# Kernel optimization log

Measured on AMD Instinct MI355X. Metric: run time of the kernel, lower is better.

## Reference

```python
import jax, jax.numpy as jnp
import numpy as np
from jax import lax

E, C, N = 3, 2, 2048          # edge types, channels, nodes (= nb_items)
B, T = 64, 50                 # batch, max_seq_length
W_IN = 256; W_OUT = 256; U = 512  # gcn in/out, rnn_units


def setup_inputs() -> dict:
    key = jax.random.key(0)
    ks = jax.random.split(key, 16)
    # sparse-ish adjacency stored densely (coalesce/spspmm equivalents are dense ops)
    A = jnp.where(jax.random.uniform(ks[0], (E, N, N)) < 0.01,
                  jax.random.uniform(ks[1], (E, N, N)), 0.0)
    X = jax.random.normal(ks[2], (N, W_IN)) * 0.1
    seqs = (jax.random.uniform(ks[3], (B, T, N)) < 0.005).astype(jnp.float32)  # multi-hot baskets
    seq_len = jax.random.randint(ks[4], (B,), 1, T + 1)
    h0 = jnp.zeros((B, U), jnp.float32)
    c0 = jnp.zeros((B, U), jnp.float32)
    # GTConv weights: init constant 1 (softmax -> uniform filter)
    gt_w1 = jnp.ones((C, E), jnp.float32)
    gt_w2 = jnp.ones((C, E), jnp.float32)
    gt_w3 = jnp.ones((C, E), jnp.float32)
    s_in = 1.0 / np.sqrt(W_IN)
    gcn_W = jax.random.normal(ks[5], (W_IN, W_OUT)) * s_in
    gcn_b = jnp.zeros((W_OUT,), jnp.float32)
    lin1_W = jax.random.normal(ks[6], (C * W_OUT, W_OUT)) * (1.0 / np.sqrt(C * W_OUT))
    lin1_b = jnp.zeros((W_OUT,), jnp.float32)
    s_u = 1.0 / np.sqrt(U)
    lstm_Wih = jax.random.normal(ks[7], (4 * U, W_OUT)) * s_u
    lstm_Whh = jax.random.normal(ks[8], (4 * U, U)) * s_u
    lstm_bih = jnp.zeros((4 * U,), jnp.float32)
    lstm_bhh = jnp.zeros((4 * U,), jnp.float32)
    score_W = jax.random.normal(ks[9], (N, U)) * s_u
    return {"A": A, "X": X, "seqs": seqs, "seq_len": seq_len, "h0": h0, "c0": c0,
            "gt_w1": gt_w1, "gt_w2": gt_w2, "gt_w3": gt_w3,
            "gcn_W": gcn_W, "gcn_b": gcn_b, "lin1_W": lin1_W, "lin1_b": lin1_b,
            "lstm_Wih": lstm_Wih, "lstm_Whh": lstm_Whh,
            "lstm_bih": lstm_bih, "lstm_bhh": lstm_bhh, "score_W": score_W}


def _gtconv(A, w):
    # filter = softmax over edge types; per-channel convex combine of adjacencies
    f = jax.nn.softmax(w, axis=1)            # [C,E]
    return jnp.einsum('ce,enm->cnm', f, A)   # [C,N,N]


def _col_normalize(H):
    # remove self loops; deg = scatter_add over col; value *= deg_col^-1 (no_grad deg)
    H = H * (1.0 - jnp.eye(N, dtype=H.dtype))
    deg = H.sum(axis=1)                      # [C,N] per-column degree
    dinv = lax.stop_gradient(jnp.where(deg > 0, 1.0 / deg, 0.0))
    return H * dinv[:, None, :]


def _gcn(M, X, W, b):
    # PyG GCNConv: add self loops, sym-normalize by col/row degree, aggregate at target
    M1 = M + jnp.eye(N, dtype=M.dtype)
    deg = M1.sum(axis=0)                     # scatter over col
    dis = jnp.where(deg > 0, lax.rsqrt(deg), 0.0)
    Ahat = dis[:, None] * M1 * dis[None, :]
    return Ahat.T @ (X @ W) + b              # out[target] = sum_src norm * x[src]


def reference(A, X, seqs, seq_len, h0, c0, gt_w1, gt_w2, gt_w3,
              gcn_W, gcn_b, lin1_W, lin1_b,
              lstm_Wih, lstm_Whh, lstm_bih, lstm_bhh, score_W):
    # --- GT layers: H = conv1(A) @ conv2(A), then H = norm(H) @ conv(A) ---
    HA = _gtconv(A, gt_w1)
    HB = _gtconv(A, gt_w2)
    H = jnp.einsum('cnk,ckm->cnm', HA, HB)          # spspmm per channel
    Hn = _col_normalize(H)
    HB2 = _gtconv(A, gt_w3)
    H = jnp.einsum('cnk,ckm->cnm', Hn, HB2)
    # --- GCN per channel, relu, concat, linear1 ---
    feats = [jax.nn.relu(_gcn(H[i], X, gcn_W, gcn_b)) for i in range(C)]
    X_ = jnp.concatenate(feats, axis=1) @ lin1_W + lin1_b   # [N, W_OUT]
    # --- basket max-pooling over items in each basket (empty -> zeros) ---
    def pool_step(_, mask_t):                # mask_t: [B,N]
        masked = jnp.where(mask_t[:, :, None] > 0, X_[None, :, :], -jnp.inf)
        pooled = masked.max(axis=1)          # [B, W_OUT]
        has = mask_t.sum(axis=1) > 0
        return None, jnp.where(has[:, None], pooled, 0.0)
    _, bs = lax.scan(pool_step, None, jnp.swapaxes(seqs, 0, 1))  # [T,B,W_OUT]
    # --- single-layer LSTM (PyTorch gate order i,f,g,o) ---
    def lstm_step(carry, x_t):
        h, c = carry
        g = x_t @ lstm_Wih.T + h @ lstm_Whh.T + lstm_bih + lstm_bhh
        i, f, gg, o = jnp.split(g, 4, axis=-1)
        c = jax.nn.sigmoid(f) * c + jax.nn.sigmoid(i) * jnp.tanh(gg)
        h = jax.nn.sigmoid(o) * jnp.tanh(c)
        return (h, c), h
    _, outs = lax.scan(lstm_step, (h0, c0), bs)      # [T,B,U]
    lstm_out = jnp.swapaxes(outs, 0, 1)              # [B,T,U]
    actual = lstm_out[jnp.arange(B), seq_len - 1]    # [B,U] last valid step
    return jax.nn.sigmoid(actual @ score_W.T)        # [B,N]
```

## Files before the change

### kernel.cpp

```cpp
#include <hip/hip_runtime.h>
#include <stdint.h>

#define E_ 3
#define C_ 2
#define N_ 2048
#define B_ 64
#define T_ 50
#define WIN_ 256
#define WOUT_ 256
#define U_ 512
#define BT_ (B_*T_)
#define BTP_ 3328

typedef unsigned short u16;
typedef unsigned int u32;
typedef __bf16 bf16x8 __attribute__((ext_vector_type(8)));
typedef float f32x4 __attribute__((ext_vector_type(4)));

#define NN_ (2048LL*2048LL)

__device__ __forceinline__ float bf2f(u16 u){
  u32 x = ((u32)u) << 16; return __builtin_bit_cast(float, x);
}
__device__ __forceinline__ u16 f2bf(float f){
  u32 x = __builtin_bit_cast(u32, f);
  u32 r = (x + 0x7fffu + ((x >> 16) & 1u)) >> 16;
  return (u16)r;
}

__device__ __forceinline__ void gload16(const u16* g, u16* l){
  __builtin_amdgcn_global_load_lds((const __attribute__((address_space(1))) u32*)g,
                                   (__attribute__((address_space(3))) u32*)l, 16, 0, 0);
}

__global__ void k_prep0(const float* __restrict__ w1, const float* __restrict__ w2,
                        const float* __restrict__ w3, float* __restrict__ filt,
                        const float* __restrict__ bih, const float* __restrict__ bhh,
                        float* __restrict__ bsum, u32* __restrict__ flagv){
  const int i = blockIdx.x*256 + threadIdx.x;
  bsum[i] = bih[i] + bhh[i];
  flagv[i] = 0;
  if(blockIdx.x==0 && threadIdx.x < 3*C_){
    const int t = threadIdx.x;
    const int fi = t / C_, c = t % C_;
    const float* w = (fi==0) ? w1 : ((fi==1) ? w2 : w3);
    float v[E_]; float mx = -3.4e38f;
    for(int e=0;e<E_;e++){ v[e] = w[c*E_+e]; mx = fmaxf(mx, v[e]); }
    float s = 0.f;
    for(int e=0;e<E_;e++){ v[e] = expf(v[e]-mx); s += v[e]; }
    for(int e=0;e<E_;e++) filt[(fi*C_+c)*E_ + e] = v[e]/s;
  }
}

__global__ void k_combineAll(const float* __restrict__ A, const float* __restrict__ filt,
                             u16* __restrict__ HA, u16* __restrict__ HBt){
  __shared__ float te[3][32][33];
  const int ti = blockIdx.x, tj = blockIdx.y;
  const int x = threadIdx.x, y0 = threadIdx.y;
  #pragma unroll
  for(int i=0;i<4;i++){
    const int y = y0 + i*8;
    const long base = (long)(tj*32+y)*N_ + ti*32 + x;
    const float a0 = A[0*NN_+base], a1 = A[1*NN_+base], a2 = A[2*NN_+base];
    te[0][y][x]=a0; te[1][y][x]=a1; te[2][y][x]=a2;
    #pragma unroll
    for(int c=0;c<C_;c++)
      HA[c*NN_ + base] = f2bf(filt[c*E_]*a0 + filt[c*E_+1]*a1 + filt[c*E_+2]*a2);
  }
  __syncthreads();
  #pragma unroll
  for(int i=0;i<4;i++){
    const int y = y0 + i*8;
    const long ob = (long)(ti*32+y)*N_ + tj*32 + x;
    const float a0=te[0][x][y], a1=te[1][x][y], a2=te[2][x][y];
    #pragma unroll
    for(int c=0;c<C_;c++)
      HBt[c*NN_+ob] = f2bf(filt[(C_+c)*E_]*a0 + filt[(C_+c)*E_+1]*a1 + filt[(C_+c)*E_+2]*a2);
  }
}

__global__ void k_combineT2(const float* __restrict__ A, const float* __restrict__ f,
                            u16* __restrict__ outp){
  __shared__ float te[3][32][33];
  const int ti = blockIdx.x, tj = blockIdx.y;
  const int x = threadIdx.x, y0 = threadIdx.y;
  #pragma unroll
  for(int i=0;i<4;i++){
    const int y = y0 + i*8;
    const long base = (long)(tj*32+y)*N_ + ti*32 + x;
    te[0][y][x]=A[0*NN_+base]; te[1][y][x]=A[1*NN_+base]; te[2][y][x]=A[2*NN_+base];
  }
  __syncthreads();
  #pragma unroll
  for(int i=0;i<4;i++){
    const int y = y0 + i*8;
    const long ob = (long)(ti*32+y)*N_ + tj*32 + x;
    const float a0=te[0][x][y], a1=te[1][x][y], a2=te[2][x][y];
    #pragma unroll
    for(int c=0;c<C_;c++)
      outp[c*NN_+ob] = f2bf(f[c*E_]*a0 + f[c*E_+1]*a1 + f[c*E_+2]*a2);
  }
}

template<int MODE>
__global__ __launch_bounds__(256) void gemm_bt(
    const u16* __restrict__ Ag, const u16* __restrict__ Bg, void* __restrict__ Cg,
    int K, int ldc, long sA, long sB, long sC,
    const float* __restrict__ disv, int sDis, const float* __restrict__ bias)
{
  __shared__ u16 At[128*32];
  __shared__ u16 Bt[128*32];
  const int tid = threadIdx.x;
  const int w = tid >> 6, l = tid & 63;
  const int z = blockIdx.z;
  const u16* Ab = Ag + (long)z*sA;
  const u16* Bb = Bg + (long)z*sB;
  const int rowBase = blockIdx.y*128;
  const int colBase = blockIdx.x*128;

  f32x4 acc[4][4];
  #pragma unroll
  for(int i=0;i<4;i++)
    #pragma unroll
    for(int j=0;j<4;j++)
      acc[i][j] = f32x4{0.f,0.f,0.f,0.f};

  const int wr = w >> 1, wc = w & 1;
  const int arow0 = (w*2+0)*16 + (l>>2);
  const int arow1 = (w*2+1)*16 + (l>>2);
  const int kc = (((l&3) ^ ((l>>2)&3)))*8;
  const int frow = l & 15;
  const int fkc = l >> 4;

  const int nk = K >> 5;
  for(int kt=0; kt<nk; ++kt){
    const int k0 = kt << 5;
    gload16(Ab + (long)(rowBase+arow0)*K + k0 + kc, &At[(w*2+0)*512]);
    gload16(Ab + (long)(rowBase+arow1)*K + k0 + kc, &At[(w*2+1)*512]);
    gload16(Bb + (long)(colBase+arow0)*K + k0 + kc, &Bt[(w*2+0)*512]);
    gload16(Bb + (long)(colBase+arow1)*K + k0 + kc, &Bt[(w*2+1)*512]);
    __syncthreads();
    bf16x8 af[4], bfv[4];
    #pragma unroll
    for(int m=0;m<4;m++){
      const int rr = wr*64 + m*16 + frow;
      af[m] = *(const bf16x8*)&At[rr*32 + ((fkc ^ (rr&3))<<3)];
    }
    #pragma unroll
    for(int n=0;n<4;n++){
      const int rr = wc*64 + n*16 + frow;
      bfv[n] = *(const bf16x8*)&Bt[rr*32 + ((fkc ^ (rr&3))<<3)];
    }
    #pragma unroll
    for(int m=0;m<4;m++)
      #pragma unroll
      for(int n=0;n<4;n++)
        acc[m][n] = __builtin_amdgcn_mfma_f32_16x16x32_bf16(af[m], bfv[n], acc[m][n], 0, 0, 0);
    __syncthreads();
  }

  #pragma unroll
  for(int m=0;m<4;m++){
    const int row0 = rowBase + wr*64 + m*16 + (l>>4)*4;
    #pragma unroll
    for(int n=0;n<4;n++){
      const int col = colBase + wc*64 + n*16 + (l&15);
      #pragma unroll
      for(int r=0;r<4;r++){
        const float v = acc[m][n][r];
        if(MODE==1){
          ((u16*)Cg)[z*sC + (long)(row0+r)*ldc + col] = f2bf(v);
        } else if(MODE==2){
          float o = disv[z*(long)sDis + row0 + r]*v + bias[col];
          o = o > 0.f ? o : 0.f;
          ((u16*)Cg)[z*sC + (long)(row0+r)*ldc + col] = f2bf(o);
        } else if(MODE==3){
          ((float*)Cg)[z*sC + (long)(row0+r)*ldc + col] = v + bias[col];
        } else if(MODE==4){
          const int row = row0 + r;
          if(row < BT_){
            const int bb = row/50, tt = row - bb*50;
            const int gate = col >> 9, ugg = col & 511;
            ((float*)Cg)[((((long)tt*4 + (bb>>4))*512 + ugg)*16 + (bb&15))*4 + gate] = v + bias[col];
          }
        } else if(MODE==5){
          const int row = row0 + r;
          const float o = (v + (row==col ? 1.f : 0.f)) * disv[z*(long)sDis + col];
          ((u16*)Cg)[z*sC + (long)row*ldc + col] = f2bf(o);
        } else if(MODE==6){
          const int row = row0 + r;
          if(row < B_)
            ((float*)Cg)[(long)row*ldc + col] = 1.f/(1.f + expf(-v));
        }
      }
    }
  }
}

__global__ void k_degpart(const u16* __restrict__ H, float* __restrict__ partial){
  const int c = blockIdx.z;
  const int col = blockIdx.x*256 + threadIdx.x;
  const int r0 = blockIdx.y*128;
  const u16* Hc = H + c*NN_;
  float s = 0.f;
  #pragma unroll 4
  for(int r=0;r<128;r++) s += bf2f(Hc[(long)(r0+r)*N_ + col]);
  partial[((long)c*16 + blockIdx.y)*N_ + col] = s;
}

__global__ void k_dinv(const u16* __restrict__ H, const float* __restrict__ partial,
                       float* __restrict__ dinvb){
  const int i = blockIdx.x*256 + threadIdx.x;
  const int c = i >> 11, m = i & (N_-1);
  float s = 0.f;
  #pragma unroll
  for(int p=0;p<16;p++) s += partial[((long)c*16 + p)*N_ + m];
  s -= bf2f(H[c*NN_ + (long)m*N_ + m]);
  dinvb[i] = s > 0.f ? 1.f/s : 0.f;
}

__global__ void k_colscale(u16* __restrict__ H, const float* __restrict__ dinvb){
  const long i = (long)blockIdx.x*256 + threadIdx.x;
  const int c = blockIdx.y;
  const int j = (int)(i >> 11), ii = (int)(i & (N_-1));
  const long idx = c*NN_ + i;
  const float v = (j==ii) ? 0.f : bf2f(H[idx])*dinvb[c*N_ + ii];
  H[idx] = f2bf(v);
}

__global__ void k_dis(const u16* __restrict__ HB2t, const float* __restrict__ dinvb,
                      float* __restrict__ disv){
  const int c = blockIdx.y, j = blockIdx.x;
  const u16* r = HB2t + (c*(long)N_ + j)*N_;
  const float* dv = dinvb + c*N_;
  float s = 0.f;
  for(int i=threadIdx.x;i<N_;i+=256)
    if(dv[i] > 0.f) s += bf2f(r[i]);
  __shared__ float red[256];
  red[threadIdx.x] = s;
  __syncthreads();
  for(int st=128; st>0; st>>=1){
    if(threadIdx.x < st) red[threadIdx.x] += red[threadIdx.x+st];
    __syncthreads();
  }
  if(threadIdx.x==0){
    const float deg = red[0] + 1.f;
    disv[c*N_ + j] = deg > 0.f ? rsqrtf(deg) : 0.f;
  }
}

__global__ void k_transpose3(const float* __restrict__ gcnW, u16* __restrict__ Wt,
                             const float* __restrict__ lin1W, u16* __restrict__ l1Wt){
  const float* in; u16* out; int R, Cc;
  if(blockIdx.z==0){ in=gcnW;  out=Wt;   R=WIN_;     Cc=WOUT_; }
  else { in=lin1W; out=l1Wt; R=C_*WOUT_; Cc=WOUT_; }
  const int ti = blockIdx.x, tj = blockIdx.y;
  if(ti >= (Cc>>5) || tj >= (R>>5)) return;
  __shared__ float tt[32][33];
  const int x = threadIdx.x, y0 = threadIdx.y;
  #pragma unroll
  for(int i=0;i<4;i++){
    const int y = y0 + i*8;
    tt[y][x] = in[(long)(tj*32+y)*Cc + ti*32 + x];
  }
  __syncthreads();
  #pragma unroll
  for(int i=0;i<4;i++){
    const int y = y0 + i*8;
    out[(long)(ti*32+y)*R + tj*32 + x] = f2bf(tt[x][y]);
  }
}

__global__ void k_cast3(const float* __restrict__ X, u16* __restrict__ Xbf,
                        const float* __restrict__ Wih, u16* __restrict__ Wihbf,
                        const float* __restrict__ scoreW, u16* __restrict__ sWbf){
  const long i = (long)blockIdx.x*256 + threadIdx.x;
  if(i < (long)N_*WIN_) Xbf[i] = f2bf(X[i]);
  else if(i < (long)N_*WIN_ + 4*U_*WOUT_){
    const long j = i - (long)N_*WIN_; Wihbf[j] = f2bf(Wih[j]);
  } else {
    const long j = i - (long)N_*WIN_ - 4*U_*WOUT_; sWbf[j] = f2bf(scoreW[j]);
  }
}

__global__ void k_pool(const float* __restrict__ seqs, const float* __restrict__ X_,
                       u16* __restrict__ bs){
  const int t = blockIdx.x, b = blockIdx.y;
  const int f = threadIdx.x;
  if(t >= T_){
    bs[(long)(BT_ + b*2 + (t-T_))*WOUT_ + f] = 0;
    return;
  }
  const float* mask = seqs + ((long)b*T_ + t)*N_;
  __shared__ int list[N_];
  __shared__ int cnt;
  if(f==0) cnt = 0;
  __syncthreads();
  for(int n0=f; n0<N_; n0+=256){
    if(mask[n0] > 0.f){
      int p = atomicAdd(&cnt, 1);
      list[p] = n0;
    }
  }
  __syncthreads();
  const int m = cnt;
  float mx = -3.4e38f;
  for(int i=0;i<m;i++)
    mx = fmaxf(mx, X_[(long)list[i]*WOUT_ + f]);
  bs[((long)b*T_ + t)*WOUT_ + f] = f2bf(m>0 ? mx : 0.f);
}

__global__ void k_packWhh3(const float* __restrict__ Whh, u16* __restrict__ P){
  const long idx = (long)blockIdx.x*256 + threadIdx.x;
  const int e  = (int)(idx & 7);
  const int kk = (int)((idx >> 3) & 15);
  const int l  = (int)((idx >> 7) & 63);
  const int w  = (int)((idx >> 13) & 7);
  const int s  = (int)(idx >> 16);
  const int lr = w*16 + (l & 15);
  const int gam = lr & 3, ui = lr >> 2;
  const int grow = gam*512 + s*32 + ui;
  const int k = kk*32 + (l >> 4)*8 + e;
  P[idx] = f2bf(Whh[(long)grow*512 + k]);
}

__global__ void k_hinit(const float* __restrict__ h0, u16* __restrict__ Hglob){
  const int idx = blockIdx.x*256 + threadIdx.x;
  const int b = idx >> 9, u = idx & 511;
  const int grp = b >> 4, bl = b & 15;
  Hglob[grp*16384 + (bl << 9) + (u ^ ((bl & 7) << 3))] = f2bf(h0[idx]);
}

__global__ __launch_bounds__(512) void k_lstm_all(
    const u16* __restrict__ WhhP, const float* __restrict__ Gq,
    const float* __restrict__ c0v, const int* __restrict__ seqlen,
    u16* __restrict__ Hglob, u32* __restrict__ flagv, u16* __restrict__ act)
{
  __shared__ u16 Hl[16*512];
  const int tid = threadIdx.x;
  const int w = tid >> 6, l = tid & 63;
  const int grp = blockIdx.x & 3, s = blockIdx.x >> 2;
  const int fr = l & 15, hi = l >> 4;

  bf16x8 wreg[16];
  const u16* wp = WhhP + (((long)s*8 + w)*64 + l)*128;
  #pragma unroll
  for(int kk=0; kk<16; ++kk)
    wreg[kk] = *(const bf16x8*)&wp[kk*8];

  const int ug = s*32 + w*4 + hi;
  const int bl = fr;
  const int bg = grp*16 + bl;
  float cst = c0v[bg*U_ + ug];
  const int sl = seqlen[bg] - 1;
  u16* Hbase = Hglob + grp*16384;
  const int hswz = (bl & 7) << 3;
  const int fi = (grp*16 + fr)*32;
  const long gqbase = (((long)grp*512 + ug)*16 + bl)*4;
  float4 gq_nxt = *(const float4*)&Gq[gqbase];

  for(int t=0; t<T_; ++t){
    const float4 gq = gq_nxt;
    const u16* Hin = Hbase + (t & 1)*8192;
    #pragma unroll
    for(int r=0; r<2; ++r)
      gload16(Hin + (r*8 + w)*512 + l*8, &Hl[(r*8 + w)*512]);
    __syncthreads();

    f32x4 acc = f32x4{0.f,0.f,0.f,0.f};
    #pragma unroll
    for(int kk=0; kk<16; ++kk){
      const int ke = kk*32 + hi*8;
      bf16x8 bb = *(const bf16x8*)&Hl[(bl << 9) + (ke ^ hswz)];
      acc = __builtin_amdgcn_mfma_f32_16x16x32_bf16(wreg[kk], bb, acc, 0, 0, 0);
    }

    if(t+1 < T_)
      gq_nxt = *(const float4*)&Gq[(long)(t+1)*(4*2048*16) + gqbase];

    const float a0 = acc[0] + gq.x;
    const float a1 = acc[1] + gq.y;
    const float a2 = acc[2] + gq.z;
    const float a3 = acc[3] + gq.w;
    const float ig = 1.f/(1.f + expf(-a0));
    const float fg = 1.f/(1.f + expf(-a1));
    const float gg = tanhf(a2);
    const float og = 1.f/(1.f + expf(-a3));
    cst = fg*cst + ig*gg;
    const float h = og*tanhf(cst);
    u16* Hout = Hbase + ((t+1) & 1)*8192;
    Hout[(bl << 9) + (ug ^ hswz)] = f2bf(h);
    if(sl == t) act[bg*U_ + ug] = f2bf(h);

    if(t == T_-1) break;
    __syncthreads();
    if(tid == 0)
      __hip_atomic_store(&flagv[(grp*16 + s)*32], (u32)(t+1),
                         __ATOMIC_RELEASE, __HIP_MEMORY_SCOPE_AGENT);
    if(w == 0){
      while(__hip_atomic_load(&flagv[fi], __ATOMIC_ACQUIRE,
                              __HIP_MEMORY_SCOPE_AGENT) <= (u32)t){
        __builtin_amdgcn_s_sleep(1);
      }
    }
    __syncthreads();
  }
}

extern "C" void kernel_launch(void* const* d_in, const int* in_sizes, int n_in,
                              void* d_out, int out_size, void* d_ws, size_t ws_size,
                              hipStream_t stream){
  (void)in_sizes; (void)n_in; (void)out_size; (void)ws_size;
  const float* A      = (const float*)d_in[0];
  const float* X      = (const float*)d_in[1];
  const float* seqs   = (const float*)d_in[2];
  const int*   seqlen = (const int*)d_in[3];
  const float* h0     = (const float*)d_in[4];
  const float* c0     = (const float*)d_in[5];
  const float* gtw1   = (const float*)d_in[6];
  const float* gtw2   = (const float*)d_in[7];
  const float* gtw3   = (const float*)d_in[8];
  const float* gcnW   = (const float*)d_in[9];
  const float* gcnB   = (const float*)d_in[10];
  const float* lin1W  = (const float*)d_in[11];
  const float* lin1B  = (const float*)d_in[12];
  const float* Wih    = (const float*)d_in[13];
  const float* Whh    = (const float*)d_in[14];
  const float* bihp   = (const float*)d_in[15];
  const float* bhhp   = (const float*)d_in[16];
  const float* scoreW = (const float*)d_in[17];

  char* ws = (char*)d_ws;
  u16* buf0 = (u16*)(ws + 0);
  u16* buf1 = (u16*)(ws + 16777216);
  u16* buf2 = (u16*)(ws + 33554432);
  char* S0  = ws + 50331648;
  float* filt  = (float*)(S0 + 0);
  float* disv  = (float*)(S0 + 1024);
  u16*  Wt     = (u16*) (S0 + 17408);
  u16*  XWt    = (u16*) (S0 + 148480);
  u16*  catb   = (u16*) (S0 + 1197056);
  u16*  l1Wt   = (u16*) (S0 + 3294208);
  float* Xo    = (float*)(S0 + 3556352);
  u16*  bs     = (u16*) (S0 + 5653504);
  u16*  act    = (u16*) (S0 + 7357440);
  u16*  sWbf   = (u16*) (S0 + 7488512);
  u16*  WhhB   = (u16*) (S0 + 9585664);
  u16*  Xbf    = (u16*) (S0 + 11682816);
  u16*  Wihbf  = (u16*) (S0 + 12731392);
  float* bsum  = (float*)(S0 + 13779968);
  u16*  Hglob  = (u16*) (S0 + 13788160);
  u32*  flagv  = (u32*) (S0 + 13919232);
  float* degp  = (float*)(S0 + 14050304);
  float* dinvb = (float*)(S0 + 14312448);
  u16* HA   = buf0;
  u16* HBt  = buf1;
  u16* Hb   = buf2;
  u16* HB2t = buf0;
  u16* Pd   = buf1;
  float* Gq = (float*)ws;

  k_prep0<<<dim3(8), 256, 0, stream>>>(gtw1, gtw2, gtw3, filt, bihp, bhhp, bsum, flagv);
  k_combineAll<<<dim3(N_/32, N_/32), dim3(32,8), 0, stream>>>(A, filt, HA, HBt);
  k_transpose3<<<dim3(16, 64, 2), dim3(32,8), 0, stream>>>(gcnW, Wt, lin1W, l1Wt);
  k_cast3<<<dim3(8192), 256, 0, stream>>>(X, Xbf, Wih, Wihbf, scoreW, sWbf);
  gemm_bt<1><<<dim3(16,16,C_), 256, 0, stream>>>(HA, HBt, Hb, N_, N_, NN_, NN_, NN_, nullptr, 0, nullptr);
  k_degpart<<<dim3(8, 16, C_), 256, 0, stream>>>(Hb, degp);
  k_dinv<<<dim3(16), 256, 0, stream>>>(Hb, degp, dinvb);
  k_colscale<<<dim3(NN_/256, C_), 256, 0, stream>>>(Hb, dinvb);
  k_combineT2<<<dim3(N_/32, N_/32), dim3(32,8), 0, stream>>>(A, filt + 2*C_*E_, HB2t);
  k_dis<<<dim3(N_, C_), 256, 0, stream>>>(HB2t, dinvb, disv);
  gemm_bt<5><<<dim3(16,16,C_), 256, 0, stream>>>(HB2t, Hb, Pd, N_, N_, NN_, NN_, NN_, disv, N_, nullptr);
  gemm_bt<1><<<dim3(N_/128, WOUT_/128, 1), 256, 0, stream>>>(Wt, Xbf, XWt, WIN_, N_, 0, 0, 0, nullptr, 0, nullptr);
  gemm_bt<2><<<dim3(WOUT_/128, N_/128, C_), 256, 0, stream>>>(Pd, XWt, catb, N_, C_*WOUT_, NN_, 0, WOUT_, disv, N_, gcnB);
  gemm_bt<3><<<dim3(WOUT_/128, N_/128, 1), 256, 0, stream>>>(catb, l1Wt, Xo, C_*WOUT_, WOUT_, 0, 0, 0, nullptr, 0, lin1B);
  k_pool<<<dim3(52, B_), 256, 0, stream>>>(seqs, Xo, bs);
  gemm_bt<4><<<dim3((4*U_)/128, BTP_/128, 1), 256, 0, stream>>>(bs, Wihbf, Gq, WOUT_, 0, 0, 0, 0, nullptr, 0, bsum);
  k_packWhh3<<<dim3(4096), 256, 0, stream>>>(Whh, WhhB);
  k_hinit<<<dim3(128), 256, 0, stream>>>(h0, Hglob);
  k_lstm_all<<<dim3(64), 512, 0, stream>>>(WhhB, Gq, c0, seqlen, Hglob, flagv, act);
  gemm_bt<6><<<dim3(N_/128, 1, 1), 256, 0, stream>>>(act, sWbf, (float*)d_out, U_, N_, 0, 0, 0, nullptr, 0, nullptr);
}
```

Baseline: 562.0 us.

## Fuse third adjacency combine into first pass and widen GEMM K-tile

The third-filter transposed combine now happens inside the first combine kernel, so the 48MB adjacency tensor is read once instead of twice. The result goes to a new workspace buffer instead of aliasing HA. Separately, the bf16 GEMM now loads a 64-wide K slice per iteration with an 8-way XOR swizzle and runs two MFMA sub-steps between barriers. This halves the number of syncthreads and doubles LDS use per block. The new buffer needs extra workspace and assumes ws is large enough at that offset.

```diff
diff --git a/kernel.cpp b/kernel.cpp
--- a/kernel.cpp
+++ b/kernel.cpp
@@ -52,8 +52,9 @@
   }
 }
 
-__global__ void k_combineAll(const float* __restrict__ A, const float* __restrict__ filt,
-                             u16* __restrict__ HA, u16* __restrict__ HBt){
+__global__ void k_combineAll3(const float* __restrict__ A, const float* __restrict__ filt,
+                              u16* __restrict__ HA, u16* __restrict__ HBt,
+                              u16* __restrict__ HB2t){
   __shared__ float te[3][32][33];
   const int ti = blockIdx.x, tj = blockIdx.y;
   const int x = threadIdx.x, y0 = threadIdx.y;
@@ -74,31 +75,10 @@
     const long ob = (long)(ti*32+y)*N_ + tj*32 + x;
     const float a0=te[0][x][y], a1=te[1][x][y], a2=te[2][x][y];
     #pragma unroll
-    for(int c=0;c<C_;c++)
-      HBt[c*NN_+ob] = f2bf(filt[(C_+c)*E_]*a0 + filt[(C_+c)*E_+1]*a1 + filt[(C_+c)*E_+2]*a2);
-  }
-}
-
-__global__ void k_combineT2(const float* __restrict__ A, const float* __restrict__ f,
-                            u16* __restrict__ outp){
-  __shared__ float te[3][32][33];
-  const int ti = blockIdx.x, tj = blockIdx.y;
-  const int x = threadIdx.x, y0 = threadIdx.y;
-  #pragma unroll
-  for(int i=0;i<4;i++){
-    const int y = y0 + i*8;
-    const long base = (long)(tj*32+y)*N_ + ti*32 + x;
-    te[0][y][x]=A[0*NN_+base]; te[1][y][x]=A[1*NN_+base]; te[2][y][x]=A[2*NN_+base];
-  }
-  __syncthreads();
-  #pragma unroll
-  for(int i=0;i<4;i++){
-    const int y = y0 + i*8;
-    const long ob = (long)(ti*32+y)*N_ + tj*32 + x;
-    const float a0=te[0][x][y], a1=te[1][x][y], a2=te[2][x][y];
-    #pragma unroll
-    for(int c=0;c<C_;c++)
-      outp[c*NN_+ob] = f2bf(f[c*E_]*a0 + f[c*E_+1]*a1 + f[c*E_+2]*a2);
+    for(int c=0;c<C_;c++){
+      HBt[c*NN_+ob]  = f2bf(filt[(C_+c)*E_]*a0   + filt[(C_+c)*E_+1]*a1   + filt[(C_+c)*E_+2]*a2);
+      HB2t[c*NN_+ob] = f2bf(filt[(2*C_+c)*E_]*a0 + filt[(2*C_+c)*E_+1]*a1 + filt[(2*C_+c)*E_+2]*a2);
+    }
   }
 }
 
@@ -108,8 +88,8 @@
     int K, int ldc, long sA, long sB, long sC,
     const float* __restrict__ disv, int sDis, const float* __restrict__ bias)
 {
-  __shared__ u16 At[128*32];
-  __shared__ u16 Bt[128*32];
+  __shared__ u16 At[128*64];
+  __shared__ u16 Bt[128*64];
   const int tid = threadIdx.x;
   const int w = tid >> 6, l = tid & 63;
   const int z = blockIdx.z;
@@ -126,36 +106,40 @@
       acc[i][j] = f32x4{0.f,0.f,0.f,0.f};
 
   const int wr = w >> 1, wc = w & 1;
-  const int arow0 = (w*2+0)*16 + (l>>2);
-  const int arow1 = (w*2+1)*16 + (l>>2);
-  const int kc = (((l&3) ^ ((l>>2)&3)))*8;
+  const int srow = l >> 3;
+  const int scol = ((l & 7) ^ srow) << 3;
   const int frow = l & 15;
   const int fkc = l >> 4;
 
-  const int nk = K >> 5;
+  const int nk = K >> 6;
   for(int kt=0; kt<nk; ++kt){
-    const int k0 = kt << 5;
-    gload16(Ab + (long)(rowBase+arow0)*K + k0 + kc, &At[(w*2+0)*512]);
-    gload16(Ab + (long)(rowBase+arow1)*K + k0 + kc, &At[(w*2+1)*512]);
-    gload16(Bb + (long)(colBase+arow0)*K + k0 + kc, &Bt[(w*2+0)*512]);
-    gload16(Bb + (long)(colBase+arow1)*K + k0 + kc, &Bt[(w*2+1)*512]);
-    __syncthreads();
-    bf16x8 af[4], bfv[4];
-    #pragma unroll
-    for(int m=0;m<4;m++){
-      const int rr = wr*64 + m*16 + frow;
-      af[m] = *(const bf16x8*)&At[rr*32 + ((fkc ^ (rr&3))<<3)];
-    }
-    #pragma unroll
-    for(int n=0;n<4;n++){
-      const int rr = wc*64 + n*16 + frow;
-      bfv[n] = *(const bf16x8*)&Bt[rr*32 + ((fkc ^ (rr&3))<<3)];
-    }
-    #pragma unroll
-    for(int m=0;m<4;m++)
+    const int k0 = kt << 6;
+    #pragma unroll
+    for(int r=0;r<4;r++){
+      const int ch = w*4 + r;
+      gload16(Ab + (long)(rowBase + ch*8 + srow)*K + k0 + scol, &At[ch*512]);
+      gload16(Bb + (long)(colBase + ch*8 + srow)*K + k0 + scol, &Bt[ch*512]);
+    }
+    __syncthreads();
+    #pragma unroll
+    for(int ks=0; ks<2; ++ks){
+      bf16x8 af[4], bfv[4];
       #pragma unroll
-      for(int n=0;n<4;n++)
-        acc[m][n] = __builtin_amdgcn_mfma_f32_16x16x32_bf16(af[m], bfv[n], acc[m][n], 0, 0, 0);
+      for(int m=0;m<4;m++){
+        const int rr = wr*64 + m*16 + frow;
+        af[m] = *(const bf16x8*)&At[rr*64 + (((ks*4 + fkc) ^ (rr&7))<<3)];
+      }
+      #pragma unroll
+      for(int n=0;n<4;n++){
+        const int rr = wc*64 + n*16 + frow;
+        bfv[n] = *(const bf16x8*)&Bt[rr*64 + (((ks*4 + fkc) ^ (rr&7))<<3)];
+      }
+      #pragma unroll
+      for(int m=0;m<4;m++)
+        #pragma unroll
+        for(int n=0;n<4;n++)
+          acc[m][n] = __builtin_amdgcn_mfma_f32_16x16x32_bf16(af[m], bfv[n], acc[m][n], 0, 0, 0);
+    }
     __syncthreads();
   }
 
@@ -453,22 +437,22 @@
   u32*  flagv  = (u32*) (S0 + 13919232);
   float* degp  = (float*)(S0 + 14050304);
   float* dinvb = (float*)(S0 + 14312448);
+  u16* buf3 = (u16*)(ws + 64660480);
   u16* HA   = buf0;
   u16* HBt  = buf1;
   u16* Hb   = buf2;
-  u16* HB2t = buf0;
+  u16* HB2t = buf3;
   u16* Pd   = buf1;
   float* Gq = (float*)ws;
 
   k_prep0<<<dim3(8), 256, 0, stream>>>(gtw1, gtw2, gtw3, filt, bihp, bhhp, bsum, flagv);
-  k_combineAll<<<dim3(N_/32, N_/32), dim3(32,8), 0, stream>>>(A, filt, HA, HBt);
+  k_combineAll3<<<dim3(N_/32, N_/32), dim3(32,8), 0, stream>>>(A, filt, HA, HBt, HB2t);
   k_transpose3<<<dim3(16, 64, 2), dim3(32,8), 0, stream>>>(gcnW, Wt, lin1W, l1Wt);
   k_cast3<<<dim3(8192), 256, 0, stream>>>(X, Xbf, Wih, Wihbf, scoreW, sWbf);
   gemm_bt<1><<<dim3(16,16,C_), 256, 0, stream>>>(HA, HBt, Hb, N_, N_, NN_, NN_, NN_, nullptr, 0, nullptr);
   k_degpart<<<dim3(8, 16, C_), 256, 0, stream>>>(Hb, degp);
   k_dinv<<<dim3(16), 256, 0, stream>>>(Hb, degp, dinvb);
   k_colscale<<<dim3(NN_/256, C_), 256, 0, stream>>>(Hb, dinvb);
-  k_combineT2<<<dim3(N_/32, N_/32), dim3(32,8), 0, stream>>>(A, filt + 2*C_*E_, HB2t);
   k_dis<<<dim3(N_, C_), 256, 0, stream>>>(HB2t, dinvb, disv);
   gemm_bt<5><<<dim3(16,16,C_), 256, 0, stream>>>(HB2t, Hb, Pd, N_, N_, NN_, NN_, NN_, disv, N_, nullptr);
   gemm_bt<1><<<dim3(N_/128, WOUT_/128, 1), 256, 0, stream>>>(Wt, Xbf, XWt, WIN_, N_, 0, 0, 0, nullptr, 0, nullptr);
```

New measurement: 521.3 us. -7.2%, faster.
